# Kernel optimization log

Hardware: AMD Instinct MI355X
Metric: run time of the kernel (lower is better)

## Reference

```python
import jax, jax.numpy as jnp
import numpy as np

B, S, D_MODEL, H = 4, 2048, 1024, 16
DEPTH = D_MODEL // H  # 64


def setup_inputs() -> dict:
    key = jax.random.key(0)
    ks = jax.random.split(key, 12)
    inp = {
        "v": jax.random.normal(ks[0], (B, S, D_MODEL), jnp.float32),
        "k": jax.random.normal(ks[1], (B, S, D_MODEL), jnp.float32),
        "q": jax.random.normal(ks[2], (B, S, D_MODEL), jnp.float32),
        "mask": jnp.zeros((B, 1, 1, S), jnp.int32),  # unused by the layer
        # Dense(d_model) params (glorot-ish scale)
        "wq": jax.random.normal(ks[3], (D_MODEL, D_MODEL), jnp.float32) / np.sqrt(D_MODEL),
        "bq": jnp.zeros((D_MODEL,), jnp.float32),
        "wk": jax.random.normal(ks[4], (D_MODEL, D_MODEL), jnp.float32) / np.sqrt(D_MODEL),
        "bk": jnp.zeros((D_MODEL,), jnp.float32),
        "wv": jax.random.normal(ks[5], (D_MODEL, D_MODEL), jnp.float32) / np.sqrt(D_MODEL),
        "bv": jnp.zeros((D_MODEL,), jnp.float32),
        # global attention weights: [max_seq_len, 1], stddev=0.1
        "gqw": 0.1 * jax.random.normal(ks[6], (S, 1), jnp.float32),
        "gkw": 0.1 * jax.random.normal(ks[7], (S, 1), jnp.float32),
        "wo": jax.random.normal(ks[8], (D_MODEL, D_MODEL), jnp.float32) / np.sqrt(D_MODEL),
        "bo": jnp.zeros((D_MODEL,), jnp.float32),
    }
    return inp


def _split_heads(x):
    # [B, S, D] -> [B, H, S, depth]
    Bc = x.shape[0]
    return x.reshape(Bc, -1, H, DEPTH).transpose(0, 2, 1, 3)


def reference(v, k, q, mask, wq, bq, wk, bk, wv, bv, gqw, gkw, wo, bo):
    # QKV projections
    qh = _split_heads(q @ wq + bq)  # [B, H, S, depth]
    kh = _split_heads(k @ wk + bk)
    vh = _split_heads(v @ wv + bv)
    # Fastformer additive attention: mul -> seq-sum -> mul -> seq-sum -> mul -> add
    qh = qh * gqw                          # gqw [S,1] broadcasts over [B,H,S,depth]
    gq = jnp.sum(qh, axis=2, keepdims=True)  # global query [B,H,1,depth]
    kh = kh * gq * gkw
    gk = jnp.sum(kh, axis=2, keepdims=True)  # global key [B,H,1,depth]
    out = vh * gk + qh                       # [B,H,S,depth]
    # merge heads and output projection
    out = out.transpose(0, 2, 1, 3).reshape(out.shape[0], -1, D_MODEL)
    return out @ wo + bo
```

## Files before the change

### kernel.cpp

```cpp
#include <hip/hip_runtime.h>

#define DM 1024
#define BATCH 4
#define SEQ 2048
#define M_TOT (BATCH*SEQ)

typedef unsigned short ushort_t;
typedef __bf16 bf16x8 __attribute__((ext_vector_type(8)));
typedef float f32x4 __attribute__((ext_vector_type(4)));
typedef unsigned short u16x8 __attribute__((ext_vector_type(8)));

__device__ __forceinline__ ushort_t f2bf(float f) {
  unsigned u = __builtin_bit_cast(unsigned, f);
  u = (u + 0x7fffu + ((u >> 16) & 1u)) >> 16;
  return (ushort_t)u;
}
__device__ __forceinline__ float bf2f(ushort_t h) {
  unsigned u = ((unsigned)h) << 16;
  return __builtin_bit_cast(float, u);
}

#define GLL(gp, lp)                                                            \
  __builtin_amdgcn_global_load_lds(                                            \
      (const __attribute__((address_space(1))) unsigned int*)(const void*)(gp),\
      (__attribute__((address_space(3))) unsigned int*)(void*)(lp), 16, 0, 0)

__device__ __forceinline__ size_t src_off(int row0, int e) {
  return (size_t)(row0 + (e >> 2)) * DM + (((e & 3) ^ ((e >> 3) & 3)) * 8);
}

__global__ void k_reduce(const float* __restrict__ q, const float* __restrict__ k,
                         const float* __restrict__ v,
                         const float* __restrict__ gqw, const float* __restrict__ gkw,
                         float* __restrict__ qr, float* __restrict__ kr,
                         float* __restrict__ G,
                         ushort_t* __restrict__ qb, ushort_t* __restrict__ vb) {
  const int b = blockIdx.x, dch = blockIdx.y, sch = blockIdx.z;
  const int d = dch * 256 + threadIdx.x;
  const int s0 = sch * (SEQ / 16);
  const size_t base = ((size_t)b * SEQ + s0) * DM + d;
  const float* qp = q + base;
  const float* kp = k + base;
  const float* vp = v + base;
  float aq = 0.f, ak = 0.f;
  for (int i = 0; i < SEQ / 16; ++i) {
    const float w = gqw[s0 + i];
    const float qv = qp[(size_t)i * DM];
    aq += w * qv;
    ak += gkw[s0 + i] * kp[(size_t)i * DM];
    qb[base + (size_t)i * DM] = f2bf(w * qv);
    vb[base + (size_t)i * DM] = f2bf(vp[(size_t)i * DM]);
  }
  atomicAdd(&qr[b * DM + d], aq);
  atomicAdd(&kr[b * DM + d], ak);
  if (b == 0 && dch == 0 && threadIdx.x < SEQ / 16) {
    atomicAdd(&G[0], gqw[s0 + threadIdx.x]);
    atomicAdd(&G[1], gkw[s0 + threadIdx.x]);
  }
}

__global__ void k_gpart(const float* __restrict__ wq, const float* __restrict__ wk,
                        const float* __restrict__ qr, const float* __restrict__ kr,
                        float* __restrict__ qacc, float* __restrict__ kacc) {
  const int d = blockIdx.x * 256 + threadIdx.x;
  const int k0 = blockIdx.y * 32;
  __shared__ float sq[4][32], sk[4][32];
  if (threadIdx.x < 128) {
    const int b = threadIdx.x >> 5, kk = threadIdx.x & 31;
    sq[b][kk] = qr[b * DM + k0 + kk];
    sk[b][kk] = kr[b * DM + k0 + kk];
  }
  __syncthreads();
  float aq[4] = {0.f, 0.f, 0.f, 0.f}, ak[4] = {0.f, 0.f, 0.f, 0.f};
#pragma unroll 8
  for (int kk = 0; kk < 32; ++kk) {
    const float wqv = wq[(size_t)(k0 + kk) * DM + d];
    const float wkv = wk[(size_t)(k0 + kk) * DM + d];
#pragma unroll
    for (int b = 0; b < 4; ++b) {
      aq[b] += sq[b][kk] * wqv;
      ak[b] += sk[b][kk] * wkv;
    }
  }
#pragma unroll
  for (int b = 0; b < 4; ++b) {
    atomicAdd(&qacc[b * DM + d], aq[b]);
    atomicAdd(&kacc[b * DM + d], ak[b]);
  }
}

__global__ void k_gfin(const float* __restrict__ qacc, const float* __restrict__ kacc,
                       const float* __restrict__ bq, const float* __restrict__ bk,
                       const float* __restrict__ G, float* __restrict__ gk) {
  const int i = blockIdx.x * 256 + threadIdx.x;
  const int d = i & (DM - 1);
  const float gqv = qacc[i] + bq[d] * G[0];
  const float gkr = kacc[i] + bk[d] * G[1];
  gk[i] = gqv * gkr;
}

__global__ void k_conv(const float* __restrict__ x0, ushort_t* __restrict__ y0,
                       const float* __restrict__ x1, ushort_t* __restrict__ y1) {
  const float* x = blockIdx.y ? x1 : x0;
  ushort_t* y = blockIdx.y ? y1 : y0;
  size_t i = (size_t)blockIdx.x * 256 + threadIdx.x;
  const float4* p = (const float4*)x + i * 2;
  float4 a = p[0], b = p[1];
  u16x8 o;
  o[0] = f2bf(a.x); o[1] = f2bf(a.y); o[2] = f2bf(a.z); o[3] = f2bf(a.w);
  o[4] = f2bf(b.x); o[5] = f2bf(b.y); o[6] = f2bf(b.z); o[7] = f2bf(b.w);
  *(u16x8*)(y + i * 8) = o;
}

__global__ void k_trans(const float* __restrict__ W, ushort_t* __restrict__ T) {
  __shared__ float ls[32][33];
  const int bi = blockIdx.x, bj = blockIdx.y;
#pragma unroll
  for (int p = 0; p < 4; ++p) {
    int e = threadIdx.x + p * 256;
    int r = e >> 5, c = e & 31;
    ls[r][c] = W[(size_t)(bi * 32 + r) * DM + bj * 32 + c];
  }
  __syncthreads();
#pragma unroll
  for (int p = 0; p < 4; ++p) {
    int e = threadIdx.x + p * 256;
    int r = e >> 5, c = e & 31;
    T[(size_t)(bj * 32 + r) * DM + bi * 32 + c] = f2bf(ls[c][r]);
  }
}

__global__ void k_wog(const ushort_t* __restrict__ woT, const float* __restrict__ gk,
                      ushort_t* __restrict__ wogT) {
  const size_t i = (size_t)blockIdx.x * 256 + threadIdx.x;
  const size_t c = i * 8;
  const int j0 = (int)(c & (DM - 1));
  const int b = (int)(c >> 20);
  u16x8 wv = *(const u16x8*)(woT + (c & ((1u << 20) - 1)));
  const float4 g0 = *(const float4*)(gk + b * DM + j0);
  const float4 g1 = *(const float4*)(gk + b * DM + j0 + 4);
  float g[8] = {g0.x, g0.y, g0.z, g0.w, g1.x, g1.y, g1.z, g1.w};
  u16x8 o;
#pragma unroll
  for (int j = 0; j < 8; ++j) o[j] = f2bf(bf2f(wv[j]) * g[j]);
  *(u16x8*)(wogT + i * 8) = o;
}

__global__ void k_bias(const float* __restrict__ wo, const float* __restrict__ bq,
                       const float* __restrict__ bv, const float* __restrict__ gk,
                       float* __restrict__ qbias, float* __restrict__ vbias) {
  const int n = blockIdx.x * 256 + threadIdx.x;
  const int k0 = blockIdx.y * 32;
  float aq = 0.f, av[4] = {0.f, 0.f, 0.f, 0.f};
  for (int kk = 0; kk < 32; ++kk) {
    const float w = wo[(size_t)(k0 + kk) * DM + n];
    aq += bq[k0 + kk] * w;
    const float bw = bv[k0 + kk] * w;
#pragma unroll
    for (int b = 0; b < 4; ++b) av[b] += bw * gk[b * DM + k0 + kk];
  }
  atomicAdd(&qbias[n], aq);
#pragma unroll
  for (int b = 0; b < 4; ++b) atomicAdd(&vbias[b * DM + n], av[b]);
}

__global__ void k_small(const ushort_t* __restrict__ woT, const ushort_t* __restrict__ wogT,
                        const ushort_t* __restrict__ wqB, const ushort_t* __restrict__ wvB,
                        ushort_t* __restrict__ WqoT, ushort_t* __restrict__ WvbT) {
  __shared__ __align__(16) ushort_t lsA[3][128 * 32];
  __shared__ __align__(16) ushort_t lsB[3][128 * 32];
  const int z = blockIdx.z;
  const ushort_t* A  = z == 0 ? woT : wogT + (size_t)(z - 1) * (DM * DM);
  const ushort_t* Bt = z == 0 ? wqB : wvB;
  ushort_t* Out      = z == 0 ? WqoT : WvbT + (size_t)(z - 1) * (DM * DM);

  const int tid = threadIdx.x;
  const int w = tid >> 6, lane = tid & 63;
  const int m0 = blockIdx.x * 128, n0 = blockIdx.y * 128;
  const int wr = w >> 1, wc = w & 1;
  const int c0 = w * 2, c1 = c0 + 1;
  const int e0 = c0 * 64 + lane, e1 = c1 * 64 + lane;
  const ushort_t* gA0 = A + src_off(m0, e0);
  const ushort_t* gA1 = A + src_off(m0, e1);
  const ushort_t* gB0 = Bt + src_off(n0, e0);
  const ushort_t* gB1 = Bt + src_off(n0, e1);

  int aoff[4], boff[4];
#pragma unroll
  for (int i = 0; i < 4; ++i) {
    const int ra = wr * 64 + i * 16 + (lane & 15);
    aoff[i] = ra * 32 + (((lane >> 4) ^ ((ra >> 1) & 3)) * 8);
    const int rb = wc * 64 + i * 16 + (lane & 15);
    boff[i] = rb * 32 + (((lane >> 4) ^ ((rb >> 1) & 3)) * 8);
  }

  f32x4 acc[4][4];
#pragma unroll
  for (int i = 0; i < 4; ++i)
#pragma unroll
    for (int j = 0; j < 4; ++j) acc[i][j] = (f32x4){0.f, 0.f, 0.f, 0.f};

  auto STAGE = [&](int tt, int buf) {
    const int o = tt * 32;
    GLL(gA0 + o, &lsA[buf][c0 * 512]);
    GLL(gA1 + o, &lsA[buf][c1 * 512]);
    GLL(gB0 + o, &lsB[buf][c0 * 512]);
    GLL(gB1 + o, &lsB[buf][c1 * 512]);
  };

  STAGE(0, 0);
  STAGE(1, 1);
#pragma unroll 1
  for (int t = 0; t < 32; ++t) {
    if (t < 31) { asm volatile("s_waitcnt vmcnt(4)" ::: "memory"); }
    else        { asm volatile("s_waitcnt vmcnt(0)" ::: "memory"); }
    __builtin_amdgcn_s_barrier();
    if (t + 2 < 32) STAGE(t + 2, (t + 2) % 3);
    const int cur = t % 3;
    bf16x8 av[4], bv[4];
#pragma unroll
    for (int i = 0; i < 4; ++i) av[i] = *(const bf16x8*)(&lsA[cur][aoff[i]]);
#pragma unroll
    for (int j = 0; j < 4; ++j) bv[j] = *(const bf16x8*)(&lsB[cur][boff[j]]);
#pragma unroll
    for (int i = 0; i < 4; ++i)
#pragma unroll
      for (int j = 0; j < 4; ++j)
        acc[i][j] = __builtin_amdgcn_mfma_f32_16x16x32_bf16(av[i], bv[j], acc[i][j], 0, 0, 0);
  }

  const int lr = (lane >> 4) * 4, lc = lane & 15;
  const int rbase = m0 + wr * 64, cbase = n0 + wc * 64;
#pragma unroll
  for (int j = 0; j < 4; ++j) {
    const int col = cbase + j * 16 + lc;
#pragma unroll
    for (int i = 0; i < 4; ++i)
#pragma unroll
      for (int t = 0; t < 4; ++t)
        Out[(size_t)(rbase + i * 16 + lr + t) * DM + col] = f2bf(acc[i][j][t]);
  }
}

__global__ __launch_bounds__(512, 1)
void k_big(const ushort_t* __restrict__ qb, const ushort_t* __restrict__ vb,
           const ushort_t* __restrict__ WqoT, const ushort_t* __restrict__ WvbT,
           const float* __restrict__ gqw, const float* __restrict__ qbias,
           const float* __restrict__ vbias, const float* __restrict__ bo,
           float* __restrict__ Out) {
  __shared__ __align__(16) ushort_t lsA[3][256 * 64];
  __shared__ __align__(16) ushort_t lsB[3][128 * 64];
  const int tid = threadIdx.x;
  const int w = tid >> 6, lane = tid & 63;
  const int m0 = blockIdx.x * 256, n0 = blockIdx.y * 128;
  const int b = m0 >> 11;
  const int wr = w >> 1, wc = w & 1;

  const int subrow = lane >> 3;
  const int srcslot = (lane & 7) ^ subrow;
  size_t offA[4], offB[2];
#pragma unroll
  for (int p = 0; p < 4; ++p) {
    const int row = (4 * w + p) * 8 + subrow;
    offA[p] = (size_t)(m0 + row) * DM + srcslot * 8;
  }
#pragma unroll
  for (int p = 0; p < 2; ++p) {
    const int row = (2 * w + p) * 8 + subrow;
    offB[p] = (size_t)(n0 + row) * DM + srcslot * 8;
  }
  const ushort_t* Bv = WvbT + (size_t)b * (DM * DM);

  const int g = lane >> 4, l7 = lane & 7, l15 = lane & 15;
  int aoff0[4], aoff1[4], boff0[4], boff1[4];
#pragma unroll
  for (int i = 0; i < 4; ++i) {
    const int ra = wr * 64 + i * 16 + l15;
    aoff0[i] = ra * 64 + ((g ^ l7) * 8);
    aoff1[i] = ra * 64 + (((4 + g) ^ l7) * 8);
    const int rb = wc * 64 + i * 16 + l15;
    boff0[i] = rb * 64 + ((g ^ l7) * 8);
    boff1[i] = rb * 64 + (((4 + g) ^ l7) * 8);
  }

  f32x4 acc[4][4];
#pragma unroll
  for (int i = 0; i < 4; ++i)
#pragma unroll
    for (int j = 0; j < 4; ++j) acc[i][j] = (f32x4){0.f, 0.f, 0.f, 0.f};

  auto STAGE = [&](int tt, int buf) {
    const ushort_t* Ab;
    const ushort_t* Bb;
    int k0;
    if (tt < 16) { Ab = qb; Bb = WqoT; k0 = tt * 64; }
    else         { Ab = vb; Bb = Bv;   k0 = (tt - 16) * 64; }
#pragma unroll
    for (int p = 0; p < 4; ++p)
      GLL(Ab + offA[p] + k0, &lsA[buf][(4 * w + p) * 512]);
#pragma unroll
    for (int p = 0; p < 2; ++p)
      GLL(Bb + offB[p] + k0, &lsB[buf][(2 * w + p) * 512]);
  };

  STAGE(0, 0);
  STAGE(1, 1);
#pragma unroll 1
  for (int t = 0; t < 32; ++t) {
    if (t < 31) { asm volatile("s_waitcnt vmcnt(6)" ::: "memory"); }
    else        { asm volatile("s_waitcnt vmcnt(0)" ::: "memory"); }
    __builtin_amdgcn_s_barrier();
    if (t + 2 < 32) STAGE(t + 2, (t + 2) % 3);
    const int cur = t % 3;
    {
      bf16x8 av[4], bv[4];
#pragma unroll
      for (int i = 0; i < 4; ++i) av[i] = *(const bf16x8*)(&lsA[cur][aoff0[i]]);
#pragma unroll
      for (int j = 0; j < 4; ++j) bv[j] = *(const bf16x8*)(&lsB[cur][boff0[j]]);
#pragma unroll
      for (int i = 0; i < 4; ++i)
#pragma unroll
        for (int j = 0; j < 4; ++j)
          acc[i][j] = __builtin_amdgcn_mfma_f32_16x16x32_bf16(av[i], bv[j], acc[i][j], 0, 0, 0);
    }
    {
      bf16x8 av[4], bv[4];
#pragma unroll
      for (int i = 0; i < 4; ++i) av[i] = *(const bf16x8*)(&lsA[cur][aoff1[i]]);
#pragma unroll
      for (int j = 0; j < 4; ++j) bv[j] = *(const bf16x8*)(&lsB[cur][boff1[j]]);
#pragma unroll
      for (int i = 0; i < 4; ++i)
#pragma unroll
        for (int j = 0; j < 4; ++j)
          acc[i][j] = __builtin_amdgcn_mfma_f32_16x16x32_bf16(av[i], bv[j], acc[i][j], 0, 0, 0);
    }
  }

  const int lr = (lane >> 4) * 4, lc = lane & 15;
  const int rbase = m0 + wr * 64, cbase = n0 + wc * 64;
#pragma unroll
  for (int j = 0; j < 4; ++j) {
    const int col = cbase + j * 16 + lc;
    const float qbn = qbias[col];
    const float cb = vbias[b * DM + col] + bo[col];
#pragma unroll
    for (int i = 0; i < 4; ++i)
#pragma unroll
      for (int t = 0; t < 4; ++t) {
        const int row = rbase + i * 16 + lr + t;
        Out[(size_t)row * DM + col] = acc[i][j][t] + gqw[row & (SEQ - 1)] * qbn + cb;
      }
  }
}

extern "C" void kernel_launch(void* const* d_in, const int* in_sizes, int n_in,
                              void* d_out, int out_size, void* d_ws, size_t ws_size,
                              hipStream_t stream) {
  const float* v   = (const float*)d_in[0];
  const float* k   = (const float*)d_in[1];
  const float* q   = (const float*)d_in[2];
  const float* wq  = (const float*)d_in[4];
  const float* bq  = (const float*)d_in[5];
  const float* wk  = (const float*)d_in[6];
  const float* bk  = (const float*)d_in[7];
  const float* wv  = (const float*)d_in[8];
  const float* bv  = (const float*)d_in[9];
  const float* gqw = (const float*)d_in[10];
  const float* gkw = (const float*)d_in[11];
  const float* wo  = (const float*)d_in[12];
  const float* bo  = (const float*)d_in[13];
  float* out = (float*)d_out;
  float* wsf = (float*)d_ws;

  float* qr    = wsf + 0;
  float* kr    = wsf + 4096;
  float* qacc  = wsf + 8192;
  float* kacc  = wsf + 12288;
  float* G     = wsf + 16384;
  float* qbias = wsf + 16640;
  float* vbias = wsf + 17664;
  float* gk    = wsf + 21760;
  ushort_t* b16  = (ushort_t*)((char*)d_ws + (1 << 17));
  ushort_t* qb   = b16;
  ushort_t* vb   = qb + (size_t)M_TOT * DM;
  ushort_t* wqB  = vb + (size_t)M_TOT * DM;
  ushort_t* wvB  = wqB + (size_t)DM * DM;
  ushort_t* woT  = wvB + (size_t)DM * DM;
  ushort_t* WqoT = woT + (size_t)DM * DM;
  ushort_t* WvbT = WqoT + (size_t)DM * DM;
  ushort_t* wogT = (ushort_t*)out;

  hipMemsetAsync(d_ws, 0, 21760 * sizeof(float), stream);

  k_conv<<<dim3((DM * DM / 8) / 256, 2), 256, 0, stream>>>(wq, wqB, wv, wvB);
  k_trans<<<dim3(32, 32), 256, 0, stream>>>(wo, woT);

  k_reduce<<<dim3(BATCH, DM / 256, 16), 256, 0, stream>>>(q, k, v, gqw, gkw, qr, kr, G, qb, vb);

  k_gpart<<<dim3(DM / 256, DM / 32), 256, 0, stream>>>(wq, wk, qr, kr, qacc, kacc);
  k_gfin<<<(BATCH * DM) / 256, 256, 0, stream>>>(qacc, kacc, bq, bk, G, gk);

  k_wog<<<(BATCH * DM * DM / 8) / 256, 256, 0, stream>>>(woT, gk, wogT);
  k_bias<<<dim3(DM / 256, DM / 32), 256, 0, stream>>>(wo, bq, bv, gk, qbias, vbias);

  k_small<<<dim3(8, 8, 5), 256, 0, stream>>>(woT, wogT, wqB, wvB, WqoT, WvbT);

  k_big<<<dim3(M_TOT / 256, DM / 128), 512, 0, stream>>>(
      qb, vb, WqoT, WvbT, gqw, qbias, vbias, bo, out);
}
```

Before: 136.8 us.

## Remap k_big warps to 2x4 layout and interleave half-stage prefetch with MFMA

Changes the wave tiling in the main fused GEMM from 4x2 (64x64 per wave) to 2x4 (128x32 per wave). The global-to-LDS prefetch is split into two halves, each issued after the LDS fragment reads of its k-half, with extra barriers between halves. MFMA blocks are wrapped in s_setprio to favour matrix issue. The goal is to overlap loads with compute more finely, at the cost of more barriers and a less square per-wave tile, which raises the A-operand LDS reads per MFMA.

```diff
diff --git a/kernel.cpp b/kernel.cpp
--- a/kernel.cpp
+++ b/kernel.cpp
@@ -254,7 +254,7 @@
   const int w = tid >> 6, lane = tid & 63;
   const int m0 = blockIdx.x * 256, n0 = blockIdx.y * 128;
   const int b = m0 >> 11;
-  const int wr = w >> 1, wc = w & 1;
+  const int wr = w >> 2, wc = w & 3;
 
   const int subrow = lane >> 3;
   const int srcslot = (lane & 7) ^ subrow;
@@ -272,85 +272,99 @@
   const ushort_t* Bv = WvbT + (size_t)b * (DM * DM);
 
   const int g = lane >> 4, l7 = lane & 7, l15 = lane & 15;
-  int aoff0[4], aoff1[4], boff0[4], boff1[4];
-#pragma unroll
-  for (int i = 0; i < 4; ++i) {
-    const int ra = wr * 64 + i * 16 + l15;
-    aoff0[i] = ra * 64 + ((g ^ l7) * 8);
-    aoff1[i] = ra * 64 + (((4 + g) ^ l7) * 8);
-    const int rb = wc * 64 + i * 16 + l15;
-    boff0[i] = rb * 64 + ((g ^ l7) * 8);
-    boff1[i] = rb * 64 + (((4 + g) ^ l7) * 8);
-  }
-
-  f32x4 acc[4][4];
-#pragma unroll
-  for (int i = 0; i < 4; ++i)
-#pragma unroll
-    for (int j = 0; j < 4; ++j) acc[i][j] = (f32x4){0.f, 0.f, 0.f, 0.f};
-
-  auto STAGE = [&](int tt, int buf) {
-    const ushort_t* Ab;
-    const ushort_t* Bb;
-    int k0;
+  int aoff[2][8], boff[2][2];
+#pragma unroll
+  for (int kh = 0; kh < 2; ++kh) {
+#pragma unroll
+    for (int i = 0; i < 8; ++i) {
+      const int ra = wr * 128 + i * 16 + l15;
+      aoff[kh][i] = ra * 64 + (((kh * 4 + g) ^ l7) * 8);
+    }
+#pragma unroll
+    for (int j = 0; j < 2; ++j) {
+      const int rb = wc * 32 + j * 16 + l15;
+      boff[kh][j] = rb * 64 + (((kh * 4 + g) ^ l7) * 8);
+    }
+  }
+
+  f32x4 acc[8][2];
+#pragma unroll
+  for (int i = 0; i < 8; ++i)
+#pragma unroll
+    for (int j = 0; j < 2; ++j) acc[i][j] = (f32x4){0.f, 0.f, 0.f, 0.f};
+
+  auto SRC = [&](int tt, const ushort_t*& Ab, const ushort_t*& Bb, int& k0) {
     if (tt < 16) { Ab = qb; Bb = WqoT; k0 = tt * 64; }
     else         { Ab = vb; Bb = Bv;   k0 = (tt - 16) * 64; }
-#pragma unroll
-    for (int p = 0; p < 4; ++p)
-      GLL(Ab + offA[p] + k0, &lsA[buf][(4 * w + p) * 512]);
-#pragma unroll
-    for (int p = 0; p < 2; ++p)
-      GLL(Bb + offB[p] + k0, &lsB[buf][(2 * w + p) * 512]);
   };
-
-  STAGE(0, 0);
-  STAGE(1, 1);
+  auto STAGE_H0 = [&](int tt, int buf) {
+    const ushort_t *Ab, *Bb; int k0; SRC(tt, Ab, Bb, k0);
+    GLL(Ab + offA[0] + k0, &lsA[buf][(4 * w + 0) * 512]);
+    GLL(Ab + offA[1] + k0, &lsA[buf][(4 * w + 1) * 512]);
+    GLL(Bb + offB[0] + k0, &lsB[buf][(2 * w + 0) * 512]);
+  };
+  auto STAGE_H1 = [&](int tt, int buf) {
+    const ushort_t *Ab, *Bb; int k0; SRC(tt, Ab, Bb, k0);
+    GLL(Ab + offA[2] + k0, &lsA[buf][(4 * w + 2) * 512]);
+    GLL(Ab + offA[3] + k0, &lsA[buf][(4 * w + 3) * 512]);
+    GLL(Bb + offB[1] + k0, &lsB[buf][(2 * w + 1) * 512]);
+  };
+
+  STAGE_H0(0, 0); STAGE_H1(0, 0);
+  STAGE_H0(1, 1); STAGE_H1(1, 1);
 #pragma unroll 1
   for (int t = 0; t < 32; ++t) {
-    if (t < 31) { asm volatile("s_waitcnt vmcnt(6)" ::: "memory"); }
-    else        { asm volatile("s_waitcnt vmcnt(0)" ::: "memory"); }
-    __builtin_amdgcn_s_barrier();
-    if (t + 2 < 32) STAGE(t + 2, (t + 2) % 3);
-    const int cur = t % 3;
+    const int cur = t % 3, nb = (t + 2) % 3;
+    const bool st = (t + 2 < 32);
+    if (t < 31) { asm volatile("s_waitcnt vmcnt(6)\n\ts_barrier" ::: "memory"); }
+    else        { asm volatile("s_waitcnt vmcnt(0)\n\ts_barrier" ::: "memory"); }
     {
-      bf16x8 av[4], bv[4];
-#pragma unroll
-      for (int i = 0; i < 4; ++i) av[i] = *(const bf16x8*)(&lsA[cur][aoff0[i]]);
-#pragma unroll
-      for (int j = 0; j < 4; ++j) bv[j] = *(const bf16x8*)(&lsB[cur][boff0[j]]);
-#pragma unroll
-      for (int i = 0; i < 4; ++i)
-#pragma unroll
-        for (int j = 0; j < 4; ++j)
+      bf16x8 av[8], bv[2];
+#pragma unroll
+      for (int i = 0; i < 8; ++i) av[i] = *(const bf16x8*)(&lsA[cur][aoff[0][i]]);
+#pragma unroll
+      for (int j = 0; j < 2; ++j) bv[j] = *(const bf16x8*)(&lsB[cur][boff[0][j]]);
+      if (st) STAGE_H0(t + 2, nb);
+      __builtin_amdgcn_s_setprio(1);
+#pragma unroll
+      for (int i = 0; i < 8; ++i)
+#pragma unroll
+        for (int j = 0; j < 2; ++j)
           acc[i][j] = __builtin_amdgcn_mfma_f32_16x16x32_bf16(av[i], bv[j], acc[i][j], 0, 0, 0);
+      __builtin_amdgcn_s_setprio(0);
+      asm volatile("s_barrier" ::: "memory");
     }
     {
-      bf16x8 av[4], bv[4];
-#pragma unroll
-      for (int i = 0; i < 4; ++i) av[i] = *(const bf16x8*)(&lsA[cur][aoff1[i]]);
-#pragma unroll
-      for (int j = 0; j < 4; ++j) bv[j] = *(const bf16x8*)(&lsB[cur][boff1[j]]);
-#pragma unroll
-      for (int i = 0; i < 4; ++i)
-#pragma unroll
-        for (int j = 0; j < 4; ++j)
+      bf16x8 av[8], bv[2];
+#pragma unroll
+      for (int i = 0; i < 8; ++i) av[i] = *(const bf16x8*)(&lsA[cur][aoff[1][i]]);
+#pragma unroll
+      for (int j = 0; j < 2; ++j) bv[j] = *(const bf16x8*)(&lsB[cur][boff[1][j]]);
+      if (st) STAGE_H1(t + 2, nb);
+      __builtin_amdgcn_s_setprio(1);
+#pragma unroll
+      for (int i = 0; i < 8; ++i)
+#pragma unroll
+        for (int j = 0; j < 2; ++j)
           acc[i][j] = __builtin_amdgcn_mfma_f32_16x16x32_bf16(av[i], bv[j], acc[i][j], 0, 0, 0);
+      __builtin_amdgcn_s_setprio(0);
+      asm volatile("s_barrier" ::: "memory");
     }
   }
 
   const int lr = (lane >> 4) * 4, lc = lane & 15;
-  const int rbase = m0 + wr * 64, cbase = n0 + wc * 64;
-#pragma unroll
-  for (int j = 0; j < 4; ++j) {
+  const int rbase = m0 + wr * 128, cbase = n0 + wc * 32;
+#pragma unroll
+  for (int j = 0; j < 2; ++j) {
     const int col = cbase + j * 16 + lc;
     const float qbn = qbias[col];
     const float cb = vbias[b * DM + col] + bo[col];
 #pragma unroll
-    for (int i = 0; i < 4; ++i)
-#pragma unroll
-      for (int t = 0; t < 4; ++t) {
-        const int row = rbase + i * 16 + lr + t;
-        Out[(size_t)row * DM + col] = acc[i][j][t] + gqw[row & (SEQ - 1)] * qbn + cb;
+    for (int i = 0; i < 8; ++i)
+#pragma unroll
+      for (int r = 0; r < 4; ++r) {
+        const int row = rbase + i * 16 + lr + r;
+        Out[(size_t)row * DM + col] = acc[i][j][r] + gqw[row & (SEQ - 1)] * qbn + cb;
       }
   }
 }
```

Measured after the change: 126.2 us. -7.7%, faster.
